# Kernel tuning notes

Hardware: AMD Instinct MI355X
Metric: run time of the kernel (lower is better)

Reference implementation:

```python
import jax, jax.numpy as jnp
import numpy as np

N = 100000      # nodes
E = 1600000     # nonzeros in sparse H (avg degree 16)
IN_DIM = 128
HID = 128
OUT = 128


def setup_inputs() -> dict:
    key = jax.random.key(0)
    k = jax.random.split(key, 8)
    X = jax.random.normal(k[0], (N, IN_DIM), dtype=jnp.float32)
    H_rows = jax.random.randint(k[1], (E,), 0, N, dtype=jnp.int32)
    H_cols = jax.random.randint(k[2], (E,), 0, N, dtype=jnp.int32)
    H_vals = jax.random.uniform(k[3], (E,), dtype=jnp.float32)
    # Linear params (PyTorch: y = x @ W.T + b); store as [in, out] for x @ W
    s1 = 1.0 / np.sqrt(IN_DIM)
    s2 = 1.0 / np.sqrt(HID)
    W1 = jax.random.uniform(k[4], (IN_DIM, HID), jnp.float32, -s1, s1)
    b1 = jax.random.uniform(k[5], (HID,), jnp.float32, -s1, s1)
    W2 = jax.random.uniform(k[6], (HID, OUT), jnp.float32, -s2, s2)
    b2 = jax.random.uniform(k[7], (OUT,), jnp.float32, -s2, s2)
    return {"X": X, "H_rows": H_rows, "H_cols": H_cols, "H_vals": H_vals,
            "W1": W1, "b1": b1, "W2": W2, "b2": b2}


def _spmm(rows, cols, vals, X):
    # sparse [N,N] @ dense [N,d] via edge gather + segment-sum
    msgs = vals[:, None] * X[cols]            # [E, d]
    return jax.ops.segment_sum(msgs, rows, num_segments=N)


def reference(X, H_rows, H_cols, H_vals, W1, b1, W2, b2):
    # num_layers == 2 branch; dropout is identity (eval mode)
    h = _spmm(H_rows, H_cols, H_vals, X @ W1 + b1)   # H @ W1(X)
    h = jax.nn.relu(h)
    out = _spmm(H_rows, H_cols, H_vals, h @ W2 + b2) # H @ W2(h)
    return out
```

## Files before the change

kernel.cpp:

```cpp
#include <hip/hip_runtime.h>

#define NNODES 100000
#define DIM 128
#define BROWS 256
#define NB ((NNODES + BROWS - 1) / BROWS)
#define BCAP 5120
#define CHUNK 4096

typedef _Float16 half8 __attribute__((ext_vector_type(8)));
typedef float f32x4 __attribute__((ext_vector_type(4)));

__device__ __forceinline__ unsigned int pack_bf16x2(float lo, float hi) {
    unsigned int ul = __float_as_uint(lo);
    unsigned int uh = __float_as_uint(hi);
    ul = (ul + 0x7fffu + ((ul >> 16) & 1u)) >> 16;
    uh = (uh + 0x7fffu + ((uh >> 16) & 1u)) & 0xffff0000u;
    return uh | ul;
}

__device__ __forceinline__ void unpack_bf16x8(uint4 v, float* f) {
    f[0] = __uint_as_float(v.x << 16); f[1] = __uint_as_float(v.x & 0xffff0000u);
    f[2] = __uint_as_float(v.y << 16); f[3] = __uint_as_float(v.y & 0xffff0000u);
    f[4] = __uint_as_float(v.z << 16); f[5] = __uint_as_float(v.z & 0xffff0000u);
    f[6] = __uint_as_float(v.w << 16); f[7] = __uint_as_float(v.w & 0xffff0000u);
}

__global__ __launch_bounds__(256) void prep_w(const float* __restrict__ W1s,
                                              const float* __restrict__ W2s,
                                              _Float16* __restrict__ Wt1,
                                              _Float16* __restrict__ Wt2) {
    const int b = blockIdx.x;
    const float* __restrict__ W = (b & 4) ? W2s : W1s;
    _Float16* __restrict__ Wt = (b & 4) ? Wt2 : Wt1;
    const int base = (b & 3) * 4096;
    for (int i = threadIdx.x; i < 4096; i += 256) {
        const int e = base + i;
        const int k = e >> 7, c = e & 127;
        Wt[c * 128 + k] = (_Float16)W[e];
    }
}

template <bool IN_BF16>
__global__ __launch_bounds__(256) void gemm_mfma(const void* __restrict__ Ain,
                                                 const _Float16* __restrict__ Wt,
                                                 const float* __restrict__ bias,
                                                 unsigned short* __restrict__ Yb, int n) {
    const int t = threadIdx.x;
    const int l = t & 63;
    const int lr = l & 15;
    const int lg = l >> 4;
    const int r0 = blockIdx.x * 128 + (t >> 6) * 32;

    half8 xf[2][4];
#pragma unroll
    for (int rt = 0; rt < 2; ++rt) {
        const int row = r0 + rt * 16 + lr;
        const bool ok = row < n;
        if (IN_BF16) {
            const uint4* __restrict__ A16 = (const uint4*)Ain;
#pragma unroll
            for (int ks = 0; ks < 4; ++ks) {
                uint4 v = make_uint4(0u, 0u, 0u, 0u);
                if (ok) v = A16[(size_t)row * 16 + ks * 4 + lg];
                float f[8];
                unpack_bf16x8(v, f);
                half8 h;
#pragma unroll
                for (int j = 0; j < 8; ++j) h[j] = (_Float16)f[j];
                xf[rt][ks] = h;
            }
        } else {
            const float4* __restrict__ A4 = (const float4*)Ain;
#pragma unroll
            for (int ks = 0; ks < 4; ++ks) {
                float4 v0 = make_float4(0.f, 0.f, 0.f, 0.f);
                float4 v1 = v0;
                if (ok) {
                    v0 = A4[(size_t)row * 32 + ks * 8 + lg * 2];
                    v1 = A4[(size_t)row * 32 + ks * 8 + lg * 2 + 1];
                }
                half8 h;
                h[0] = (_Float16)v0.x; h[1] = (_Float16)v0.y;
                h[2] = (_Float16)v0.z; h[3] = (_Float16)v0.w;
                h[4] = (_Float16)v1.x; h[5] = (_Float16)v1.y;
                h[6] = (_Float16)v1.z; h[7] = (_Float16)v1.w;
                xf[rt][ks] = h;
            }
        }
    }

    const f32x4 zero4 = {0.f, 0.f, 0.f, 0.f};
    f32x4 acc[2][8];
#pragma unroll
    for (int rt = 0; rt < 2; ++rt)
#pragma unroll
        for (int ct = 0; ct < 8; ++ct) acc[rt][ct] = zero4;

    const half8* __restrict__ Wf = (const half8*)Wt;
#pragma unroll
    for (int ct = 0; ct < 8; ++ct) {
        half8 wf[4];
#pragma unroll
        for (int ks = 0; ks < 4; ++ks)
            wf[ks] = Wf[(ct * 16 + lr) * 16 + ks * 4 + lg];
#pragma unroll
        for (int ks = 0; ks < 4; ++ks) {
            acc[0][ct] = __builtin_amdgcn_mfma_f32_16x16x32_f16(wf[ks], xf[0][ks], acc[0][ct], 0, 0, 0);
            acc[1][ct] = __builtin_amdgcn_mfma_f32_16x16x32_f16(wf[ks], xf[1][ks], acc[1][ct], 0, 0, 0);
        }
    }

#pragma unroll
    for (int ct = 0; ct < 8; ++ct) {
        const int c0 = ct * 16 + lg * 4;
        const float4 bv = *(const float4*)&bias[c0];
#pragma unroll
        for (int rt = 0; rt < 2; ++rt) {
            const int row = r0 + rt * 16 + lr;
            if (row < n) {
                f32x4 a = acc[rt][ct];
                uint2 pv = make_uint2(pack_bf16x2(a[0] + bv.x, a[1] + bv.y),
                                      pack_bf16x2(a[2] + bv.z, a[3] + bv.w));
                *(uint2*)&Yb[(size_t)row * DIM + c0] = pv;
            }
        }
    }
}

__global__ __launch_bounds__(256) void pass1_bin(const int* __restrict__ rows,
                                                 const int* __restrict__ cols,
                                                 const float* __restrict__ vals,
                                                 int* __restrict__ bcnt,
                                                 int2* __restrict__ tmp, int nnz) {
    __shared__ int hist[NB];
    __shared__ int base[NB];
    __shared__ int cur[NB];
    const int t = threadIdx.x;
    const int e0 = blockIdx.x * CHUNK;
    const int e1 = min(e0 + CHUNK, nnz);

    for (int i = t; i < NB; i += 256) { hist[i] = 0; cur[i] = 0; }
    __syncthreads();

    for (int i = e0 + t; i < e1; i += 256)
        atomicAdd(&hist[rows[i] >> 8], 1);
    __syncthreads();

    for (int i = t; i < NB; i += 256)
        base[i] = (hist[i] > 0) ? atomicAdd(&bcnt[i], hist[i]) : 0;
    __syncthreads();

    for (int i = e0 + t; i < e1; i += 256) {
        const int r = rows[i];
        const int b = r >> 8;
        const int pos = base[b] + atomicAdd(&cur[b], 1);
        if (pos < BCAP)
            tmp[(size_t)b * BCAP + pos] =
                make_int2(((r & 255) << 24) | cols[i], __float_as_int(vals[i]));
    }
}

__global__ __launch_bounds__(512) void scan_buckets(const int* __restrict__ bcnt,
                                                    int* __restrict__ bbase, int nb) {
    __shared__ int s[512];
    const int t = threadIdx.x;
    const int v = (t < nb) ? bcnt[t] : 0;
    s[t] = v;
    __syncthreads();
    for (int off = 1; off < 512; off <<= 1) {
        int x = (t >= off) ? s[t - off] : 0;
        __syncthreads();
        s[t] += x;
        __syncthreads();
    }
    if (t < nb) bbase[t] = s[t] - v;
}

__global__ __launch_bounds__(256) void pass2_sort(const int2* __restrict__ tmp,
                                                  const int* __restrict__ bcnt,
                                                  const int* __restrict__ bbase,
                                                  int2* __restrict__ epack,
                                                  int* __restrict__ row_ptr,
                                                  int* __restrict__ counts, int n) {
    __shared__ int cnt[256];
    __shared__ int s[256];
    __shared__ int cur[256];
    const int b = blockIdx.x;
    const int t = threadIdx.x;
    const int row0 = b * BROWS;
    const int nrows = min(BROWS, n - row0);
    const int m = min(bcnt[b], BCAP);
    const int base = bbase[b];
    const int2* __restrict__ src = tmp + (size_t)b * BCAP;

    cnt[t] = 0;
    __syncthreads();
    for (int i = t; i < m; i += 256)
        atomicAdd(&cnt[((unsigned)src[i].x) >> 24], 1);
    __syncthreads();

    const int v = cnt[t];
    s[t] = v;
    __syncthreads();
    for (int off = 1; off < 256; off <<= 1) {
        int x = (t >= off) ? s[t - off] : 0;
        __syncthreads();
        s[t] += x;
        __syncthreads();
    }
    const int excl = s[t] - v;
    if (t < nrows) {
        row_ptr[row0 + t] = base + excl;
        counts[row0 + t] = v;
    }
    cur[t] = base + excl;
    __syncthreads();

    for (int i = t; i < m; i += 256) {
        const int2 e = src[i];
        const int rl = ((unsigned)e.x) >> 24;
        const int pos = atomicAdd(&cur[rl], 1);
        epack[pos] = make_int2(e.x & 0xFFFFFF, e.y);
    }
}

template <bool RELU_OUT, bool OUT_BF16>
__global__ __launch_bounds__(256) void spmm_csr(const int* __restrict__ row_ptr,
                                                const int* __restrict__ counts,
                                                const int2* __restrict__ epack,
                                                const unsigned short* __restrict__ Xb,
                                                void* __restrict__ out, int n) {
    const int gid = blockIdx.x * blockDim.x + threadIdx.x;
    const int r = gid >> 4;
    const int lane = gid & 15;
    if (r >= n) return;
    const int start = row_ptr[r];
    const int cnt = counts[r];
    const uint4* __restrict__ X16 = (const uint4*)Xb;
    const int2* __restrict__ ep = epack + start;

    float acc[8];
#pragma unroll
    for (int k = 0; k < 8; ++k) acc[k] = 0.f;

    int j = 0;
    for (; j + 4 <= cnt; j += 4) {
        const int2 e0 = ep[j], e1 = ep[j + 1], e2 = ep[j + 2], e3 = ep[j + 3];
        const uint4 x0 = X16[(size_t)e0.x * 16 + lane];
        const uint4 x1 = X16[(size_t)e1.x * 16 + lane];
        const uint4 x2 = X16[(size_t)e2.x * 16 + lane];
        const uint4 x3 = X16[(size_t)e3.x * 16 + lane];
        const float v0 = __int_as_float(e0.y), v1 = __int_as_float(e1.y);
        const float v2 = __int_as_float(e2.y), v3 = __int_as_float(e3.y);
        float f0[8], f1[8], f2[8], f3[8];
        unpack_bf16x8(x0, f0); unpack_bf16x8(x1, f1);
        unpack_bf16x8(x2, f2); unpack_bf16x8(x3, f3);
#pragma unroll
        for (int k = 0; k < 8; ++k)
            acc[k] += v0 * f0[k] + v1 * f1[k] + v2 * f2[k] + v3 * f3[k];
    }
    for (; j < cnt; ++j) {
        const int2 e = ep[j];
        const uint4 x = X16[(size_t)e.x * 16 + lane];
        const float v = __int_as_float(e.y);
        float f[8];
        unpack_bf16x8(x, f);
#pragma unroll
        for (int k = 0; k < 8; ++k) acc[k] += v * f[k];
    }

    if (RELU_OUT) {
#pragma unroll
        for (int k = 0; k < 8; ++k) acc[k] = fmaxf(acc[k], 0.f);
    }

    if (OUT_BF16) {
        uint4 pv = make_uint4(pack_bf16x2(acc[0], acc[1]), pack_bf16x2(acc[2], acc[3]),
                              pack_bf16x2(acc[4], acc[5]), pack_bf16x2(acc[6], acc[7]));
        ((uint4*)out)[(size_t)r * 16 + lane] = pv;
    } else {
        float* of = (float*)out;
        *(float4*)&of[(size_t)r * DIM + lane * 8]     = make_float4(acc[0], acc[1], acc[2], acc[3]);
        *(float4*)&of[(size_t)r * DIM + lane * 8 + 4] = make_float4(acc[4], acc[5], acc[6], acc[7]);
    }
}

extern "C" void kernel_launch(void* const* d_in, const int* in_sizes, int n_in,
                              void* d_out, int out_size, void* d_ws, size_t ws_size,
                              hipStream_t stream) {
    const float* X      = (const float*)d_in[0];
    const int*   H_rows = (const int*)d_in[1];
    const int*   H_cols = (const int*)d_in[2];
    const float* H_vals = (const float*)d_in[3];
    const float* W1     = (const float*)d_in[4];
    const float* b1     = (const float*)d_in[5];
    const float* W2     = (const float*)d_in[6];
    const float* b2     = (const float*)d_in[7];
    float* out = (float*)d_out;

    const int E = in_sizes[1];
    const int N = NNODES;
    const size_t bmat_bytes = (size_t)N * DIM * 2;

    const int gemm_blocks = (N + 127) / 128;
    const int p1_blocks = (E + CHUNK - 1) / CHUNK;
    const int spmm_blocks = (N * 16 + 255) / 256;

    char* p = (char*)d_ws;
    unsigned short* Yb = (unsigned short*)p;  p += bmat_bytes;
    unsigned short* hb = (unsigned short*)p;  p += bmat_bytes;
    _Float16* Wt1      = (_Float16*)p;        p += 128 * 128 * 2;
    _Float16* Wt2      = (_Float16*)p;        p += 128 * 128 * 2;
    int2* epack        = (int2*)p;            p += (size_t)E * 8;
    int2* tmp          = (int2*)p;            p += (size_t)NB * BCAP * 8;
    int*  bcnt         = (int*)p;             p += (size_t)NB * 4;
    int*  bbase        = (int*)p;             p += (size_t)NB * 4;
    int*  row_ptr      = (int*)p;             p += (size_t)N * 4;
    int*  counts       = (int*)p;             p += (size_t)N * 4;

    prep_w<<<8, 256, 0, stream>>>(W1, W2, Wt1, Wt2);

    hipMemsetAsync(bcnt, 0, (size_t)NB * 4, stream);
    pass1_bin<<<p1_blocks, 256, 0, stream>>>(H_rows, H_cols, H_vals, bcnt, tmp, E);
    scan_buckets<<<1, 512, 0, stream>>>(bcnt, bbase, NB);
    pass2_sort<<<NB, 256, 0, stream>>>(tmp, bcnt, bbase, epack, row_ptr, counts, N);

    gemm_mfma<false><<<gemm_blocks, 256, 0, stream>>>(X, Wt1, b1, Yb, N);
    spmm_csr<true, true><<<spmm_blocks, 256, 0, stream>>>(row_ptr, counts, epack, Yb, hb, N);

    gemm_mfma<true><<<gemm_blocks, 256, 0, stream>>>(hb, Wt2, b2, Yb, N);
    spmm_csr<false, false><<<spmm_blocks, 256, 0, stream>>>(row_ptr, counts, epack, Yb, out, N);
}
```

Baseline: 364.1 us.

## Fold bucket scan into pass2 and sort each row's edges by column in LDS

Removes the separate single-block scan kernel: each pass2 block now sums all preceding bucket counts itself with a block reduction. Edges are scattered into a shared-memory buffer (40 KB for BCAP int2), each thread insertion-sorts its own row's edges by column index, and the block then writes them out coalesced. Sorting by column is meant to improve gather locality in the SpMM kernels and the coalesced store replaces scattered global writes. In exchange it adds redundant prefix work per block, serial per-thread sorting, and heavy LDS use that lowers occupancy.

```diff
diff --git a/kernel.cpp b/kernel.cpp
--- a/kernel.cpp
+++ b/kernel.cpp
@@ -160,28 +160,12 @@
     }
 }
 
-__global__ __launch_bounds__(512) void scan_buckets(const int* __restrict__ bcnt,
-                                                    int* __restrict__ bbase, int nb) {
-    __shared__ int s[512];
-    const int t = threadIdx.x;
-    const int v = (t < nb) ? bcnt[t] : 0;
-    s[t] = v;
-    __syncthreads();
-    for (int off = 1; off < 512; off <<= 1) {
-        int x = (t >= off) ? s[t - off] : 0;
-        __syncthreads();
-        s[t] += x;
-        __syncthreads();
-    }
-    if (t < nb) bbase[t] = s[t] - v;
-}
-
 __global__ __launch_bounds__(256) void pass2_sort(const int2* __restrict__ tmp,
                                                   const int* __restrict__ bcnt,
-                                                  const int* __restrict__ bbase,
                                                   int2* __restrict__ epack,
                                                   int* __restrict__ row_ptr,
                                                   int* __restrict__ counts, int n) {
+    __shared__ int2 ebuf[BCAP];
     __shared__ int cnt[256];
     __shared__ int s[256];
     __shared__ int cur[256];
@@ -190,8 +174,18 @@
     const int row0 = b * BROWS;
     const int nrows = min(BROWS, n - row0);
     const int m = min(bcnt[b], BCAP);
-    const int base = bbase[b];
     const int2* __restrict__ src = tmp + (size_t)b * BCAP;
+
+    int partial = 0;
+    for (int i = t; i < b; i += 256) partial += bcnt[i];
+    s[t] = partial;
+    __syncthreads();
+    for (int off = 128; off >= 1; off >>= 1) {
+        if (t < off) s[t] += s[t + off];
+        __syncthreads();
+    }
+    const int base = s[0];
+    __syncthreads();
 
     cnt[t] = 0;
     __syncthreads();
@@ -213,15 +207,31 @@
         row_ptr[row0 + t] = base + excl;
         counts[row0 + t] = v;
     }
-    cur[t] = base + excl;
+    cur[t] = excl;
     __syncthreads();
 
     for (int i = t; i < m; i += 256) {
         const int2 e = src[i];
         const int rl = ((unsigned)e.x) >> 24;
         const int pos = atomicAdd(&cur[rl], 1);
-        epack[pos] = make_int2(e.x & 0xFFFFFF, e.y);
-    }
+        ebuf[pos] = make_int2(e.x & 0xFFFFFF, e.y);
+    }
+    __syncthreads();
+
+    {
+        const int lo = excl;
+        const int hi = s[t];
+        for (int i = lo + 1; i < hi; ++i) {
+            int2 key = ebuf[i];
+            int j = i - 1;
+            while (j >= lo && ebuf[j].x > key.x) { ebuf[j + 1] = ebuf[j]; --j; }
+            ebuf[j + 1] = key;
+        }
+    }
+    __syncthreads();
+
+    for (int i = t; i < m; i += 256)
+        epack[base + i] = ebuf[i];
 }
 
 template <bool RELU_OUT, bool OUT_BF16>
@@ -314,7 +324,6 @@
     int2* epack        = (int2*)p;            p += (size_t)E * 8;
     int2* tmp          = (int2*)p;            p += (size_t)NB * BCAP * 8;
     int*  bcnt         = (int*)p;             p += (size_t)NB * 4;
-    int*  bbase        = (int*)p;             p += (size_t)NB * 4;
     int*  row_ptr      = (int*)p;             p += (size_t)N * 4;
     int*  counts       = (int*)p;             p += (size_t)N * 4;
 
@@ -322,8 +331,7 @@
 
     hipMemsetAsync(bcnt, 0, (size_t)NB * 4, stream);
     pass1_bin<<<p1_blocks, 256, 0, stream>>>(H_rows, H_cols, H_vals, bcnt, tmp, E);
-    scan_buckets<<<1, 512, 0, stream>>>(bcnt, bbase, NB);
-    pass2_sort<<<NB, 256, 0, stream>>>(tmp, bcnt, bbase, epack, row_ptr, counts, N);
+    pass2_sort<<<NB, 256, 0, stream>>>(tmp, bcnt, epack, row_ptr, counts, N);
 
     gemm_mfma<false><<<gemm_blocks, 256, 0, stream>>>(X, Wt1, b1, Yb, N);
     spmm_csr<true, true><<<spmm_blocks, 256, 0, stream>>>(row_ptr, counts, epack, Yb, hb, N);
```

Result: slower. 405.7 us (+11.4%).
